# Performance work log

Measured on AMD Instinct MI355X. Metric: run time of the kernel, lower is better.

The kernel has to match this reference:

```python
import jax, jax.numpy as jnp
import numpy as np

NUM_FIELDS = 32  # m
EMBED = 64       # d
HIDDEN = 256     # conv output channels per layer


def setup_inputs() -> dict:
    key = jax.random.key(0)
    ks = jax.random.split(key, 8)
    m, d, H = NUM_FIELDS, EMBED, HIDDEN
    prev = [m, H // 2, H // 2]  # prev_dim entering each layer (split_half)
    x = jax.random.normal(ks[0], (1024, m, d), dtype=jnp.float32)
    W0 = jax.random.normal(ks[1], (m * prev[0], H), dtype=jnp.float32) * 0.02
    W1 = jax.random.normal(ks[2], (m * prev[1], H), dtype=jnp.float32) * 0.02
    W2 = jax.random.normal(ks[3], (m * prev[2], H), dtype=jnp.float32) * 0.02
    b0 = jnp.zeros((H,), jnp.float32)
    b1 = jnp.zeros((H,), jnp.float32)
    b2 = jnp.zeros((H,), jnp.float32)
    fc_in = H // 2 + H // 2 + H  # 512
    fc_W = jax.random.normal(ks[4], (fc_in, 1), dtype=jnp.float32) * 0.02
    fc_b = jnp.zeros((1,), jnp.float32)
    return {"x": x, "W0": W0, "b0": b0, "W1": W1, "b1": b1,
            "W2": W2, "b2": b2, "fc_W": fc_W, "fc_b": fc_b}


def _cin_forward(x, Ws, bs, fc_W, fc_b):
    num_layers = len(Ws)
    x0 = x  # (b, m, d)
    h = x
    xs = []
    for i in range(num_layers):
        b_, m, d = x0.shape
        n = h.shape[1]
        # outer product interaction: (b, m, n, d) -> flatten field pairs
        z = jnp.einsum('bmd,bnd->bmnd', x0, h).reshape(b_, m * n, d)
        # 1x1 Conv1D over channel dim (m*n): (b, k, d),(k, H) -> (b, H, d)
        y = jax.nn.relu(jnp.einsum('bkd,kh->bhd', z, Ws[i]) + bs[i][None, :, None])
        if i != num_layers - 1:  # split_half
            half = y.shape[1] // 2
            xcur, h = y[:, :half], y[:, half:]
        else:
            xcur = y
            h = y
        xs.append(xcur)
    f = jnp.concatenate(xs, axis=1)  # (b, fc_in, d)
    f = jnp.sum(f, axis=2)           # (b, fc_in)
    return f @ fc_W + fc_b           # (b, 1)


def reference(x, W0, b0, W1, b1, W2, b2, fc_W, fc_b):
    return _cin_forward(x, [W0, W1, W2], [b0, b1, b2], fc_W, fc_b)
```

## Files before the change

kernel.cpp:

```cpp
#include <hip/hip_runtime.h>

typedef __attribute__((ext_vector_type(8))) short bf16x8;
typedef __attribute__((ext_vector_type(4))) float f32x4;

__device__ __forceinline__ float bf2f(unsigned short u){
    unsigned int v = ((unsigned int)u) << 16;
    return __builtin_bit_cast(float, v);
}
__device__ __forceinline__ unsigned short f2bf(float f){
    unsigned int u = __builtin_bit_cast(unsigned int, f);
    u += 0x7FFFu + ((u >> 16) & 1u);
    return (unsigned short)(u >> 16);
}
__device__ __forceinline__ unsigned int cvt_pk_bf16(float lo, float hi){
    unsigned int r;
    asm("v_cvt_pk_bf16_f32 %0, %1, %2" : "=v"(r) : "v"(lo), "v"(hi));
    return r;
}
__device__ __forceinline__ unsigned int mulpack(unsigned int u, float xf){
    float flo = __builtin_bit_cast(float, u << 16);
    float fhi = __builtin_bit_cast(float, u & 0xffff0000u);
    return cvt_pk_bf16(xf * flo, xf * fhi);
}

__global__ void prep_wt(const float* __restrict__ W, unsigned short* __restrict__ Wt, int K){
    __shared__ float tile[64][65];
    const int k0 = blockIdx.x * 64;
    const int j0 = blockIdx.y * 64;
    const int t  = threadIdx.x;
    #pragma unroll
    for (int it = 0; it < 16; it++){
        int idx = it * 256 + t;
        int kr = idx >> 6, jc = idx & 63;
        tile[kr][jc] = W[(size_t)(k0 + kr) * 256 + j0 + jc];
    }
    __syncthreads();
    #pragma unroll
    for (int it = 0; it < 2; it++){
        int idx = it * 256 + t;
        int jr = idx >> 3, kc = (idx & 7) << 3;
        uint4 tv;
        unsigned short* ts = (unsigned short*)&tv;
        #pragma unroll
        for (int q = 0; q < 8; q++)
            ts[q] = f2bf(tile[kc + q][jr]);
        *(uint4*)(Wt + (size_t)(j0 + jr) * K + k0 + kc) = tv;
    }
}

__global__ void prep_x(const float* __restrict__ x, unsigned short* __restrict__ Xt){
    int b = blockIdx.x;
    int t = threadIdx.x;
    #pragma unroll
    for (int it = 0; it < 8; it++){
        int o = it * 256 + t;
        int d = o >> 5, m = o & 31;
        Xt[(size_t)b * 2048 + o] = f2bf(x[(size_t)b * 2048 + m * 64 + d]);
    }
}

__global__ void init_out(float* __restrict__ out, const float* __restrict__ fcb){
    int i = blockIdx.x * 256 + threadIdx.x;
    if (i < 1024) out[i] = fcb[0];
}

template<int NN, int KTOT, int JX, bool HAS_HOUT>
__global__ __launch_bounds__(512, 2) void cin_stage(
    const unsigned short* __restrict__ Xt,
    const unsigned short* __restrict__ Hin,
    const unsigned short* __restrict__ Wt,
    const float* __restrict__ bias,
    const float* __restrict__ fcW,
    unsigned short* __restrict__ Hout,
    float* __restrict__ out)
{
    constexpr int SB  = NN / 32;
    constexpr int XS  = 40;
    constexpr int ZS  = (NN == 32) ? 40 : 136;
    constexpr int XLSZ = 128 * XS;
    constexpr int HLSZ = (NN == 32) ? 0 : 128 * ZS;
    constexpr int ZMSZ = 128 * ZS;
    constexpr int NEED = XLSZ + HLSZ + 2 * ZMSZ;
    constexpr int SMSZ = NEED > 17408 ? NEED : 17408;

    __shared__ unsigned short smem[SMSZ];
    unsigned short* const Xl  = smem;
    unsigned short* const Hl  = (NN == 32) ? smem : (smem + XLSZ);
    unsigned short* const Zm0 = smem + XLSZ + HLSZ;
    unsigned short* const Zm1 = Zm0 + ZMSZ;
    unsigned short* const Yl  = smem;

    const int t    = threadIdx.x;
    const int lane = t & 63;
    const int w    = t >> 6;
    const int li   = lane & 15;
    const int lq   = lane >> 4;
    const int bpair = blockIdx.x;

    {
        const int c  = t >> 2;
        const int b  = bpair * 2 + (c >> 6);
        const int d  = c & 63;
        const int mh = (t & 3) << 3;
        uint4 xq = *(const uint4*)(Xt + ((size_t)b << 11) + (d << 5) + mh);
        *(uint4*)(Xl + c * XS + mh) = xq;
        if (NN == 128){
            const int nh = (t & 3) << 5;
            const uint4* hsrc = (const uint4*)(Hin + (size_t)((b << 6) + d) * 128 + nh);
            #pragma unroll
            for (int q = 0; q < 4; q++){
                uint4 hv = hsrc[q];
                *(uint4*)(Hl + c * ZS + nh + q * 8) = hv;
            }
        }
    }

    const int bc = t >> 2;
    const int bn0 = (t & 3) * (NN / 4);
    auto build = [&](int m, unsigned short* zdst){
        float xf = bf2f(Xl[bc * XS + m]);
        #pragma unroll
        for (int q8 = 0; q8 < NN / 32; q8++){
            uint4 hv = *(const uint4*)(Hl + bc * ZS + bn0 + q8 * 8);
            uint4 zv;
            zv.x = mulpack(hv.x, xf);
            zv.y = mulpack(hv.y, xf);
            zv.z = mulpack(hv.z, xf);
            zv.w = mulpack(hv.w, xf);
            *(uint4*)(zdst + bc * ZS + bn0 + q8 * 8) = zv;
        }
    };

    const unsigned short* wrow = Wt + (size_t)((w << 5) + li) * KTOT + (lq << 3);
    auto aload = [&](bf16x8 (&A)[2][SB], int mm){
        #pragma unroll
        for (int jt = 0; jt < 2; jt++)
            #pragma unroll
            for (int s = 0; s < SB; s++)
                A[jt][s] = *(const bf16x8*)(wrow + (size_t)jt * 16 * KTOT + (mm * SB + s) * 32);
    };

    f32x4 acc[2][8];
    #pragma unroll
    for (int jt = 0; jt < 2; jt++)
        #pragma unroll
        for (int ct = 0; ct < 8; ct++)
            acc[jt][ct] = (f32x4){0.f, 0.f, 0.f, 0.f};

    auto mfma_phase = [&](const unsigned short* zp, bf16x8 (&Ar)[2][SB]){
        bf16x8 Bf[2][8];
        #pragma unroll
        for (int ct = 0; ct < 8; ct++)
            Bf[0][ct] = *(const bf16x8*)(zp + ((ct << 4) + li) * ZS + (lq << 3));
        #pragma unroll
        for (int s = 0; s < SB; s++){
            if (s + 1 < SB){
                #pragma unroll
                for (int ct = 0; ct < 8; ct++)
                    Bf[(s + 1) & 1][ct] = *(const bf16x8*)(zp + ((ct << 4) + li) * ZS + ((s + 1) << 5) + (lq << 3));
            }
            #pragma unroll
            for (int ct = 0; ct < 8; ct++)
                #pragma unroll
                for (int jt = 0; jt < 2; jt++)
                    acc[jt][ct] = __builtin_amdgcn_mfma_f32_16x16x32_bf16(
                        Ar[jt][s], Bf[s & 1][ct], acc[jt][ct], 0, 0, 0);
        }
    };

    __syncthreads();
    bf16x8 Aa[2][SB], Ab[2][SB];
    build(0, Zm0);
    aload(Aa, 0);
    __syncthreads();

    for (int m = 0; m < 32; m += 2){
        aload(Ab, m + 1);
        mfma_phase(Zm0, Aa);
        build(m + 1, Zm1);
        __syncthreads();
        aload(Aa, (m + 2 < 32) ? m + 2 : 31);
        mfma_phase(Zm1, Ab);
        if (m + 2 < 32) build(m + 2, Zm0);
        __syncthreads();
    }

    float pfc0 = 0.f, pfc1 = 0.f;
    #pragma unroll
    for (int jt = 0; jt < 2; jt++){
        const int jb = (w << 5) + (jt << 4) + (lq << 2);
        float bv[4], fv[4];
        #pragma unroll
        for (int r = 0; r < 4; r++){
            int j = jb + r;
            bv[r] = bias[j];
            fv[r] = (j < JX) ? fcW[j] : 0.f;
        }
        #pragma unroll
        for (int ct = 0; ct < 8; ct++){
            f32x4 f = acc[jt][ct];
            int c = (ct << 4) + li;
            float ps = 0.f;
            #pragma unroll
            for (int r = 0; r < 4; r++){
                float y = f[r] + bv[r];
                y = y > 0.f ? y : 0.f;
                ps += fv[r] * y;
                if (HAS_HOUT){
                    int j = jb + r;
                    if (j >= 128)
                        Yl[(j - 128) * 136 + c] = f2bf(y);
                }
            }
            if (ct < 4) pfc0 += ps; else pfc1 += ps;
        }
    }
    #pragma unroll
    for (int off = 32; off; off >>= 1){
        pfc0 += __shfl_xor(pfc0, off, 64);
        pfc1 += __shfl_xor(pfc1, off, 64);
    }
    if (lane == 0){
        atomicAdd(out + bpair * 2 + 0, pfc0);
        atomicAdd(out + bpair * 2 + 1, pfc1);
    }

    if (HAS_HOUT){
        __syncthreads();
        const int c  = t >> 2;
        const int nh = (t & 3) << 5;
        unsigned short* gdst = Hout + (size_t)(bpair * 128 + c) * 128 + nh;
        #pragma unroll
        for (int i8 = 0; i8 < 4; i8++){
            uint4 tv;
            unsigned short* tmp2 = (unsigned short*)&tv;
            #pragma unroll
            for (int q = 0; q < 8; q++)
                tmp2[q] = Yl[(nh + i8 * 8 + q) * 136 + c];
            *(uint4*)(gdst + i8 * 8) = tv;
        }
    }
}

extern "C" void kernel_launch(void* const* d_in, const int* in_sizes, int n_in,
                              void* d_out, int out_size, void* d_ws, size_t ws_size,
                              hipStream_t stream){
    const float* x   = (const float*)d_in[0];
    const float* W0  = (const float*)d_in[1];
    const float* b0  = (const float*)d_in[2];
    const float* W1  = (const float*)d_in[3];
    const float* b1  = (const float*)d_in[4];
    const float* W2  = (const float*)d_in[5];
    const float* b2  = (const float*)d_in[6];
    const float* fcW = (const float*)d_in[7];
    const float* fcb = (const float*)d_in[8];
    float* out = (float*)d_out;

    char* ws = (char*)d_ws;
    unsigned short* Xt  = (unsigned short*)(ws);
    unsigned short* Wt0 = (unsigned short*)(ws + 4194304);
    unsigned short* Wt1 = (unsigned short*)(ws + 4718592);
    unsigned short* Wt2 = (unsigned short*)(ws + 6815744);
    unsigned short* H0  = (unsigned short*)(ws + 8912896);
    unsigned short* H1  = (unsigned short*)(ws + 25690112);

    prep_wt<<<dim3(16, 4), 256, 0, stream>>>(W0, Wt0, 1024);
    prep_wt<<<dim3(64, 4), 256, 0, stream>>>(W1, Wt1, 4096);
    prep_wt<<<dim3(64, 4), 256, 0, stream>>>(W2, Wt2, 4096);
    prep_x <<<1024, 256, 0, stream>>>(x, Xt);
    init_out<<<4, 256, 0, stream>>>(out, fcb);

    cin_stage< 32, 1024, 128, true ><<<512, 512, 0, stream>>>(Xt, Xt, Wt0, b0, fcW,       H0, out);
    cin_stage<128, 4096, 128, true ><<<512, 512, 0, stream>>>(Xt, H0, Wt1, b1, fcW + 128, H1, out);
    cin_stage<128, 4096, 256, false><<<512, 512, 0, stream>>>(Xt, H1, Wt2, b2, fcW + 256, nullptr, out);
}
```

Measured before the change: 395.9 us.

## Halve block size, give each wave 64 output channels, single-buffer Z tile

Blocks shrink from 512 to 256 threads, and each wave now computes 64 output channels (4 MFMA row tiles) instead of 32. This doubles register-level reuse of each B fragment read from LDS. The double-buffered Z tile and the software pipeline that overlapped the next build and A load with MFMAs are replaced by a single buffer with two barriers per m step. This saves LDS but serialises build and MFMA work, and the larger accumulator and A-fragment arrays raise register pressure.

Result: no change. 402.2 us (+1.6%).

```diff
diff --git a/kernel.cpp b/kernel.cpp
--- a/kernel.cpp
+++ b/kernel.cpp
@@ -65,7 +65,7 @@
 }
 
 template<int NN, int KTOT, int JX, bool HAS_HOUT>
-__global__ __launch_bounds__(512, 2) void cin_stage(
+__global__ __launch_bounds__(256, 2) void cin_stage(
     const unsigned short* __restrict__ Xt,
     const unsigned short* __restrict__ Hin,
     const unsigned short* __restrict__ Wt,
@@ -80,15 +80,14 @@
     constexpr int XLSZ = 128 * XS;
     constexpr int HLSZ = (NN == 32) ? 0 : 128 * ZS;
     constexpr int ZMSZ = 128 * ZS;
-    constexpr int NEED = XLSZ + HLSZ + 2 * ZMSZ;
+    constexpr int NEED = XLSZ + HLSZ + ZMSZ;
     constexpr int SMSZ = NEED > 17408 ? NEED : 17408;
 
     __shared__ unsigned short smem[SMSZ];
-    unsigned short* const Xl  = smem;
-    unsigned short* const Hl  = (NN == 32) ? smem : (smem + XLSZ);
-    unsigned short* const Zm0 = smem + XLSZ + HLSZ;
-    unsigned short* const Zm1 = Zm0 + ZMSZ;
-    unsigned short* const Yl  = smem;
+    unsigned short* const Xl = smem;
+    unsigned short* const Hl = (NN == 32) ? smem : (smem + XLSZ);
+    unsigned short* const Zm = smem + XLSZ + HLSZ;
+    unsigned short* const Yl = smem;
 
     const int t    = threadIdx.x;
     const int lane = t & 63;
@@ -98,97 +97,94 @@
     const int bpair = blockIdx.x;
 
     {
-        const int c  = t >> 2;
+        const int c  = t >> 1;
         const int b  = bpair * 2 + (c >> 6);
         const int d  = c & 63;
-        const int mh = (t & 3) << 3;
-        uint4 xq = *(const uint4*)(Xt + ((size_t)b << 11) + (d << 5) + mh);
-        *(uint4*)(Xl + c * XS + mh) = xq;
+        const int half = t & 1;
+        const int mh = half << 4;
+        const uint4* xsrc = (const uint4*)(Xt + ((size_t)b << 11) + (d << 5) + mh);
+        uint4 x0 = xsrc[0], x1 = xsrc[1];
+        *(uint4*)(Xl + c * XS + mh)     = x0;
+        *(uint4*)(Xl + c * XS + mh + 8) = x1;
         if (NN == 128){
-            const int nh = (t & 3) << 5;
+            const int nh = half << 6;
             const uint4* hsrc = (const uint4*)(Hin + (size_t)((b << 6) + d) * 128 + nh);
             #pragma unroll
-            for (int q = 0; q < 4; q++){
+            for (int q = 0; q < 8; q++){
                 uint4 hv = hsrc[q];
                 *(uint4*)(Hl + c * ZS + nh + q * 8) = hv;
             }
         }
     }
 
-    const int bc = t >> 2;
-    const int bn0 = (t & 3) * (NN / 4);
-    auto build = [&](int m, unsigned short* zdst){
+    const int bc = t & 127;
+    const int bh = t >> 7;
+    constexpr int CPT = (NN == 128) ? 8 : 2;
+    auto build = [&](int m){
         float xf = bf2f(Xl[bc * XS + m]);
         #pragma unroll
-        for (int q8 = 0; q8 < NN / 32; q8++){
-            uint4 hv = *(const uint4*)(Hl + bc * ZS + bn0 + q8 * 8);
+        for (int j = 0; j < CPT; j++){
+            int off = (bh * CPT + j) << 3;
+            uint4 hv = *(const uint4*)(Hl + bc * ZS + off);
             uint4 zv;
             zv.x = mulpack(hv.x, xf);
             zv.y = mulpack(hv.y, xf);
             zv.z = mulpack(hv.z, xf);
             zv.w = mulpack(hv.w, xf);
-            *(uint4*)(zdst + bc * ZS + bn0 + q8 * 8) = zv;
+            *(uint4*)(Zm + bc * ZS + off) = zv;
         }
     };
 
-    const unsigned short* wrow = Wt + (size_t)((w << 5) + li) * KTOT + (lq << 3);
-    auto aload = [&](bf16x8 (&A)[2][SB], int mm){
-        #pragma unroll
-        for (int jt = 0; jt < 2; jt++)
+    const unsigned short* wrow = Wt + (size_t)((w << 6) + li) * KTOT + (lq << 3);
+    bf16x8 A[4][SB];
+    auto aload = [&](int m){
+        #pragma unroll
+        for (int jt = 0; jt < 4; jt++)
             #pragma unroll
             for (int s = 0; s < SB; s++)
-                A[jt][s] = *(const bf16x8*)(wrow + (size_t)jt * 16 * KTOT + (mm * SB + s) * 32);
+                A[jt][s] = *(const bf16x8*)(wrow + (size_t)jt * 16 * KTOT + (m * SB + s) * 32);
     };
 
-    f32x4 acc[2][8];
-    #pragma unroll
-    for (int jt = 0; jt < 2; jt++)
+    f32x4 acc[4][8];
+    #pragma unroll
+    for (int jt = 0; jt < 4; jt++)
         #pragma unroll
         for (int ct = 0; ct < 8; ct++)
             acc[jt][ct] = (f32x4){0.f, 0.f, 0.f, 0.f};
 
-    auto mfma_phase = [&](const unsigned short* zp, bf16x8 (&Ar)[2][SB]){
-        bf16x8 Bf[2][8];
-        #pragma unroll
-        for (int ct = 0; ct < 8; ct++)
-            Bf[0][ct] = *(const bf16x8*)(zp + ((ct << 4) + li) * ZS + (lq << 3));
+    __syncthreads();
+    build(0);
+    aload(0);
+    __syncthreads();
+
+    for (int m = 0; m < 32; m++){
         #pragma unroll
         for (int s = 0; s < SB; s++){
-            if (s + 1 < SB){
-                #pragma unroll
-                for (int ct = 0; ct < 8; ct++)
-                    Bf[(s + 1) & 1][ct] = *(const bf16x8*)(zp + ((ct << 4) + li) * ZS + ((s + 1) << 5) + (lq << 3));
-            }
+            bf16x8 Bf[8];
+            #pragma unroll
+            for (int ct = 0; ct < 8; ct++)
+                Bf[ct] = *(const bf16x8*)(Zm + ((ct << 4) + li) * ZS + (s << 5) + (lq << 3));
             #pragma unroll
             for (int ct = 0; ct < 8; ct++)
                 #pragma unroll
-                for (int jt = 0; jt < 2; jt++)
+                for (int jt = 0; jt < 4; jt++)
                     acc[jt][ct] = __builtin_amdgcn_mfma_f32_16x16x32_bf16(
-                        Ar[jt][s], Bf[s & 1][ct], acc[jt][ct], 0, 0, 0);
-        }
-    };
-
-    __syncthreads();
-    bf16x8 Aa[2][SB], Ab[2][SB];
-    build(0, Zm0);
-    aload(Aa, 0);
-    __syncthreads();
-
-    for (int m = 0; m < 32; m += 2){
-        aload(Ab, m + 1);
-        mfma_phase(Zm0, Aa);
-        build(m + 1, Zm1);
+                        A[jt][s], Bf[ct], acc[jt][ct], 0, 0, 0);
+        }
         __syncthreads();
-        aload(Aa, (m + 2 < 32) ? m + 2 : 31);
-        mfma_phase(Zm1, Ab);
-        if (m + 2 < 32) build(m + 2, Zm0);
+        if (m < 31){
+            aload(m + 1);
+            build(m + 1);
+        }
         __syncthreads();
     }
 
+    if (HAS_HOUT) __syncthreads();
+
     float pfc0 = 0.f, pfc1 = 0.f;
     #pragma unroll
-    for (int jt = 0; jt < 2; jt++){
-        const int jb = (w << 5) + (jt << 4) + (lq << 2);
+    for (int jt = 0; jt < 4; jt++){
+        const int jb = (w << 6) + (jt << 4) + (lq << 2);
         float bv[4], fv[4];
         #pragma unroll
         for (int r = 0; r < 4; r++){
@@ -227,11 +223,11 @@
 
     if (HAS_HOUT){
         __syncthreads();
-        const int c  = t >> 2;
-        const int nh = (t & 3) << 5;
+        const int c  = t >> 1;
+        const int nh = (t & 1) << 6;
         unsigned short* gdst = Hout + (size_t)(bpair * 128 + c) * 128 + nh;
         #pragma unroll
-        for (int i8 = 0; i8 < 4; i8++){
+        for (int i8 = 0; i8 < 8; i8++){
             uint4 tv;
             unsigned short* tmp2 = (unsigned short*)&tv;
             #pragma unroll
@@ -270,7 +266,7 @@
     prep_x <<<1024, 256, 0, stream>>>(x, Xt);
     init_out<<<4, 256, 0, stream>>>(out, fcb);
 
-    cin_stage< 32, 1024, 128, true ><<<512, 512, 0, stream>>>(Xt, Xt, Wt0, b0, fcW,       H0, out);
-    cin_stage<128, 4096, 128, true ><<<512, 512, 0, stream>>>(Xt, H0, Wt1, b1, fcW + 128, H1, out);
-    cin_stage<128, 4096, 256, false><<<512, 512, 0, stream>>>(Xt, H1, Wt2, b2, fcW + 256, nullptr, out);
-}
+    cin_stage< 32, 1024, 128, true ><<<512, 256, 0, stream>>>(Xt, Xt, Wt0, b0, fcW,       H0, out);
+    cin_stage<128, 4096, 128, true ><<<512, 256, 0, stream>>>(Xt, H0, Wt1, b1, fcW + 128, H1, out);
+    cin_stage<128, 4096, 256, false><<<512, 256, 0, stream>>>(Xt, H1, Wt2, b2, fcW + 256, nullptr, out);
+}
```
